# Kernel optimization log

Measured on AMD Instinct MI355X. Metric: run time of the kernel, lower is better.

## Reference

```python
import jax, jax.numpy as jnp
import numpy as np

NEG_INF = -1e9  # matches masked_fill value in torch code
LRELU_ALPHA = 0.2


def setup_inputs() -> dict:
    key = jax.random.key(0)
    k1, k2, k3, k4 = jax.random.split(key, 4)
    B, N, F_IN, H, DK = 4, 2048, 128, 4, 32
    x = jax.random.normal(k1, (B, N, F_IN), dtype=jnp.float32)
    adj = jax.random.randint(k2, (B, N, N), 0, 2, dtype=jnp.int32)
    # xavier-ish scaled params
    W = jax.random.normal(k3, (H, F_IN, DK), dtype=jnp.float32) * (1.0 / np.sqrt(F_IN))
    a = jax.random.normal(k4, (H, 2 * DK, 1), dtype=jnp.float32) * (1.0 / np.sqrt(2 * DK))
    return {"x": x, "adj": adj, "W": W, "a": a}


def reference(x, adj, W, a):
    B, N, _ = x.shape
    H, _, DK = W.shape
    # h: (B, H, N, DK)
    h = jnp.einsum('bni,hio->bhno', x, W)
    # Split attention vector: e[b,h,i,j] = h_i.a_l + h_j.a_r  (avoids O(N^2 * 2d) concat)
    a_l = a[:, :DK, 0]   # (H, DK)
    a_r = a[:, DK:, 0]   # (H, DK)
    el = jnp.einsum('bhnd,hd->bhn', h, a_l)  # (B, H, N)
    er = jnp.einsum('bhnd,hd->bhn', h, a_r)  # (B, H, N)
    e = el[:, :, :, None] + er[:, :, None, :]          # (B, H, N, N)
    e = jax.nn.leaky_relu(e, negative_slope=LRELU_ALPHA)
    e = jnp.where(adj[:, None, :, :] == 0, NEG_INF, e)
    alpha = jax.nn.softmax(e, axis=-1)                 # dropout is identity (eval)
    h_prime = jnp.einsum('bhij,bhjd->bhid', alpha, h)  # (B, H, N, DK)
    # torch code does h_prime.view(B, N, -1) on contiguous (B,H,N,DK): raw reshape
    out = h_prime.reshape(B, N, H * DK)
    return out
```

## Files before the change

### kernel.cpp

```cpp
#include <hip/hip_runtime.h>
#include <stdint.h>

#define LOG2E 1.4426950408889634f

typedef __bf16 v8bf __attribute__((ext_vector_type(8)));
typedef float v16f __attribute__((ext_vector_type(16)));

static constexpr int B = 4, N = 2048, FIN = 128, H = 4, DK = 32;
static constexpr int IT = N / 32;

__device__ __forceinline__ float exp2_fast(float x) {
#if __has_builtin(__builtin_amdgcn_exp2f)
  return __builtin_amdgcn_exp2f(x);
#else
  float r;
  asm("v_exp_f32 %0, %1" : "=v"(r) : "v"(x));
  return r;
#endif
}

__device__ __forceinline__ unsigned int bf16_rne(float f) {
  unsigned int u = __builtin_bit_cast(unsigned int, f);
  u += 0x7FFFu + ((u >> 16) & 1u);
  return u >> 16;
}

__global__ __launch_bounds__(256) void k_prep(const float* __restrict__ x,
                                              const float* __restrict__ W,
                                              unsigned short* __restrict__ xb,
                                              unsigned short* __restrict__ wtb) {
  int idx = blockIdx.x * 256 + threadIdx.x;
  constexpr int TX = B * N * FIN;
  if (idx < TX) {
    xb[idx] = (unsigned short)bf16_rne(x[idx]);
  } else {
    int j = idx - TX;
    int h = j >> 12, r = j & 4095, d = r >> 7, f = r & 127;
    wtb[j] = (unsigned short)bf16_rne(W[(h * FIN + f) * DK + d]);
  }
}

__global__ __launch_bounds__(256) void k_pack(const int* __restrict__ adj,
                                              unsigned int* __restrict__ adjb) {
  int wid = (blockIdx.x * 256 + threadIdx.x) >> 6;
  int lane = threadIdx.x & 63;
  const int* p = adj + (size_t)wid * 256 + lane;
  unsigned long long m0 = __ballot(p[0] != 0);
  unsigned long long m1 = __ballot(p[64] != 0);
  unsigned long long m2 = __ballot(p[128] != 0);
  unsigned long long m3 = __ballot(p[192] != 0);
  if (lane == 0) {
    uint4 v0 = {(unsigned)m0, (unsigned)(m0 >> 32), (unsigned)m1, (unsigned)(m1 >> 32)};
    uint4 v1 = {(unsigned)m2, (unsigned)(m2 >> 32), (unsigned)m3, (unsigned)(m3 >> 32)};
    uint4* dst = (uint4*)(adjb + (size_t)wid * 8);
    dst[0] = v0;
    dst[1] = v1;
  }
}

__global__ __launch_bounds__(256) void k_hproj(const unsigned short* __restrict__ xb,
                                               const unsigned short* __restrict__ wtb,
                                               const float* __restrict__ a,
                                               unsigned short* __restrict__ h_t,
                                               float* __restrict__ el,
                                               float* __restrict__ er) {
  int blk = blockIdx.x;
  int b = blk >> 6, it = blk & 63;
  int tid = threadIdx.x;
  int head = tid >> 6, lane = tid & 63;
  int lrow = lane & 31, kh = lane >> 5;
  int bh = b * H + head;
  int n = it * 32 + lrow;
  const unsigned short* xp = xb + (b * N + n) * FIN + kh * 8;
  const unsigned short* wp = wtb + (head * DK + lrow) * FIN + kh * 8;
  v16f acc = {};
#pragma unroll
  for (int s = 0; s < FIN / 16; ++s) {
    v8bf av = __builtin_bit_cast(v8bf, *(const int4*)(wp + s * 16));
    v8bf bv = __builtin_bit_cast(v8bf, *(const int4*)(xp + s * 16));
    acc = __builtin_amdgcn_mfma_f32_32x32x16_bf16(av, bv, acc, 0, 0, 0);
  }
  float pel = 0.f, per = 0.f;
#pragma unroll
  for (int r = 0; r < 16; ++r) {
    int d = (r & 3) + 8 * (r >> 2) + 4 * kh;
    float hv = acc[r];
    h_t[(bh * DK + d) * N + n] = (unsigned short)bf16_rne(hv);
    pel = fmaf(hv, a[head * 2 * DK + d], pel);
    per = fmaf(hv, a[head * 2 * DK + DK + d], per);
  }
  pel += __shfl_xor(pel, 32);
  per += __shfl_xor(per, 32);
  if (kh == 0) {
    el[bh * N + n] = pel * LOG2E;
    er[bh * N + n] = per * LOG2E;
  }
}

__global__ __launch_bounds__(1024, 4) void k_attn(const unsigned int* __restrict__ adjb,
                                                  const unsigned short* __restrict__ h_t,
                                                  const float* __restrict__ el,
                                                  const float* __restrict__ er,
                                                  float* __restrict__ out) {
  __shared__ float part[H][1024];
  __shared__ float lsh[H][32];
  int blk = blockIdx.x;
  int b = blk >> 6, it = blk & 63;
  int tid = threadIdx.x;
  int wave = tid >> 6;
  int head = wave & 3, jq = wave >> 2;
  int lane = tid & 63, lrow = lane & 31, kh = lane >> 5;
  int ig = it * 32 + lrow, bh = b * H + head;

  part[tid >> 8][tid & 255] = 0.f;
  part[tid >> 8][256 + (tid & 255)] = 0.f;
  part[tid >> 8][512 + (tid & 255)] = 0.f;
  part[tid >> 8][768 + (tid & 255)] = 0.f;
  if (tid < H * 32) lsh[tid >> 5][tid & 31] = 0.f;

  float eli = el[bh * N + ig];
  int j0 = jq * 512 + kh * 8;
  const float* erp = er + bh * N + j0;
  const unsigned short* hp = h_t + (size_t)(bh * DK + lrow) * N + j0;

  const uint4* abp = (const uint4*)(adjb + (size_t)(b * N + ig) * 64 + jq * 16);
  uint4 ab0 = abp[0], ab1 = abp[1], ab2 = abp[2], ab3 = abp[3];
  unsigned adw[16] = {ab0.x, ab0.y, ab0.z, ab0.w, ab1.x, ab1.y, ab1.z, ab1.w,
                      ab2.x, ab2.y, ab2.z, ab2.w, ab3.x, ab3.y, ab3.z, ab3.w};
  int shkh = kh * 8;

  __syncthreads();

  v16f acc = {};
  float lsum = 0.f;
  float4 Ea = *(const float4*)erp;
  float4 Eb = *(const float4*)(erp + 4);
  int4 Hb = *(const int4*)hp;
#pragma unroll
  for (int s = 0; s < 32; ++s) {
    float4 ea = Ea, eb = Eb;
    int4 hb = Hb;
    if (s + 1 < 32) {
      int o = (s + 1) * 16;
      Ea = *(const float4*)(erp + o);
      Eb = *(const float4*)(erp + o + 4);
      Hb = *(const int4*)(hp + o);
    }
    unsigned mb = (adw[s >> 1] >> (((s & 1) * 16) + shkh)) & 0xFFu;
    float ev[8] = {ea.x, ea.y, ea.z, ea.w, eb.x, eb.y, eb.z, eb.w};
    unsigned ub[8];
#pragma unroll
    for (int k = 0; k < 8; ++k) {
      float tt = eli + ev[k];
      tt = fmaxf(tt, 0.2f * tt);
      float pv = exp2_fast(tt);
      unsigned u = __builtin_bit_cast(unsigned, pv) & 0xFFFF0000u;
      u = (mb & (1u << k)) ? u : 0u;
      ub[k] = u;
      lsum += __builtin_bit_cast(float, u);
    }
    unsigned u0 = __builtin_amdgcn_perm(ub[1], ub[0], 0x07060302u);
    unsigned u1 = __builtin_amdgcn_perm(ub[3], ub[2], 0x07060302u);
    unsigned u2 = __builtin_amdgcn_perm(ub[5], ub[4], 0x07060302u);
    unsigned u3 = __builtin_amdgcn_perm(ub[7], ub[6], 0x07060302u);
    uint4 au = {u0, u1, u2, u3};
    v8bf av = __builtin_bit_cast(v8bf, au);
    v8bf hv = __builtin_bit_cast(v8bf, hb);
    acc = __builtin_amdgcn_mfma_f32_32x32x16_bf16(av, hv, acc, 0, 0, 0);
  }

  lsum += __shfl_xor(lsum, 32);
  if (lane < 32) atomicAdd(&lsh[head][lane], lsum);
#pragma unroll
  for (int r = 0; r < 16; ++r) {
    int rowl = (r & 3) + 8 * (r >> 2) + 4 * kh;
    atomicAdd(&part[head][rowl * 32 + lrow], acc[r]);
  }
  __syncthreads();

  int e = tid * 4;
  int rh = e >> 10;
  int ri = (e >> 5) & 31;
  int rd = e & 31;
  float4 s4 = *(const float4*)&part[rh][ri * 32 + rd];
  float inv = 1.0f / lsh[rh][ri];
  float4 o;
  o.x = s4.x * inv;
  o.y = s4.y * inv;
  o.z = s4.z * inv;
  o.w = s4.w * inv;
  *(float4*)&out[(size_t)((b * H + rh) * N + it * 32 + ri) * DK + rd] = o;
}

extern "C" void kernel_launch(void* const* d_in, const int* in_sizes, int n_in,
                              void* d_out, int out_size, void* d_ws, size_t ws_size,
                              hipStream_t stream) {
  const float* x = (const float*)d_in[0];
  const int* adj = (const int*)d_in[1];
  const float* W = (const float*)d_in[2];
  const float* a = (const float*)d_in[3];
  float* out = (float*)d_out;
  char* ws = (char*)d_ws;

  unsigned short* h_t = (unsigned short*)(ws);
  float* el = (float*)(ws + 0x200000);
  float* er = (float*)(ws + 0x220000);
  unsigned short* wtb = (unsigned short*)(ws + 0x240000);
  unsigned int* adjb = (unsigned int*)(ws + 0x250000);
  unsigned short* xb = (unsigned short*)(ws + 0x450000);

  hipLaunchKernelGGL(k_pack, dim3(B * N * N / 256 / 4), dim3(256), 0, stream, adj, adjb);
  hipLaunchKernelGGL(k_prep, dim3((B * N * FIN + H * DK * FIN) / 256), dim3(256), 0, stream,
                     x, W, xb, wtb);
  hipLaunchKernelGGL(k_hproj, dim3(B * IT), dim3(256), 0, stream, xb, wtb, a, h_t, el, er);
  hipLaunchKernelGGL(k_attn, dim3(B * IT), dim3(1024), 0, stream, adjb, h_t, el, er, out);
}
```

Baseline: 146.5 us.

## Fuse adjacency mask read into attention kernel and drop bit-packing pass

Removes the separate kernel that packed the int32 adjacency matrix into bitmasks. The attention kernel now reads raw adjacency rows itself, double-buffering them alongside the h tiles, and stages the per-head er vector in shared memory. Blocks shrink to 512 threads, so each wave covers 1024 columns. The two column-halves are combined with ordered shared-memory writes instead of LDS atomics. This saves one launch and the bitmask write/read round trip. In exchange, each block's four head waves load the same int32 adjacency rows separately, and more registers go to in-flight loads.

New measurement: 238.3 us. 62.7% more time.

```diff
diff --git a/kernel.cpp b/kernel.cpp
--- a/kernel.cpp
+++ b/kernel.cpp
@@ -37,24 +37,6 @@
     int j = idx - TX;
     int h = j >> 12, r = j & 4095, d = r >> 7, f = r & 127;
     wtb[j] = (unsigned short)bf16_rne(W[(h * FIN + f) * DK + d]);
-  }
-}
-
-__global__ __launch_bounds__(256) void k_pack(const int* __restrict__ adj,
-                                              unsigned int* __restrict__ adjb) {
-  int wid = (blockIdx.x * 256 + threadIdx.x) >> 6;
-  int lane = threadIdx.x & 63;
-  const int* p = adj + (size_t)wid * 256 + lane;
-  unsigned long long m0 = __ballot(p[0] != 0);
-  unsigned long long m1 = __ballot(p[64] != 0);
-  unsigned long long m2 = __ballot(p[128] != 0);
-  unsigned long long m3 = __ballot(p[192] != 0);
-  if (lane == 0) {
-    uint4 v0 = {(unsigned)m0, (unsigned)(m0 >> 32), (unsigned)m1, (unsigned)(m1 >> 32)};
-    uint4 v1 = {(unsigned)m2, (unsigned)(m2 >> 32), (unsigned)m3, (unsigned)(m3 >> 32)};
-    uint4* dst = (uint4*)(adjb + (size_t)wid * 8);
-    dst[0] = v0;
-    dst[1] = v1;
   }
 }
 
@@ -97,13 +79,14 @@
   }
 }
 
-__global__ __launch_bounds__(1024, 4) void k_attn(const unsigned int* __restrict__ adjb,
-                                                  const unsigned short* __restrict__ h_t,
-                                                  const float* __restrict__ el,
-                                                  const float* __restrict__ er,
-                                                  float* __restrict__ out) {
-  __shared__ float part[H][1024];
-  __shared__ float lsh[H][32];
+__global__ __launch_bounds__(512, 6) void k_attn(const int* __restrict__ adj,
+                                                 const unsigned short* __restrict__ h_t,
+                                                 const float* __restrict__ el,
+                                                 const float* __restrict__ er,
+                                                 float* __restrict__ out) {
+  __shared__ float ersh[H * N];
+  __shared__ float part[H * 1024];
+  __shared__ float lsh[H * 32];
   int blk = blockIdx.x;
   int b = blk >> 6, it = blk & 63;
   int tid = threadIdx.x;
@@ -112,41 +95,34 @@
   int lane = tid & 63, lrow = lane & 31, kh = lane >> 5;
   int ig = it * 32 + lrow, bh = b * H + head;
 
-  part[tid >> 8][tid & 255] = 0.f;
-  part[tid >> 8][256 + (tid & 255)] = 0.f;
-  part[tid >> 8][512 + (tid & 255)] = 0.f;
-  part[tid >> 8][768 + (tid & 255)] = 0.f;
-  if (tid < H * 32) lsh[tid >> 5][tid & 31] = 0.f;
+  {
+    const float4* esrc = (const float4*)(er + b * H * N);
+    float4* edst = (float4*)ersh;
+#pragma unroll
+    for (int r = 0; r < 4; ++r) edst[tid + r * 512] = esrc[tid + r * 512];
+  }
+  __syncthreads();
 
   float eli = el[bh * N + ig];
-  int j0 = jq * 512 + kh * 8;
-  const float* erp = er + bh * N + j0;
+  int j0 = jq * 1024 + kh * 8;
+  const int* arow = adj + (size_t)(b * N + ig) * N + j0;
   const unsigned short* hp = h_t + (size_t)(bh * DK + lrow) * N + j0;
-
-  const uint4* abp = (const uint4*)(adjb + (size_t)(b * N + ig) * 64 + jq * 16);
-  uint4 ab0 = abp[0], ab1 = abp[1], ab2 = abp[2], ab3 = abp[3];
-  unsigned adw[16] = {ab0.x, ab0.y, ab0.z, ab0.w, ab1.x, ab1.y, ab1.z, ab1.w,
-                      ab2.x, ab2.y, ab2.z, ab2.w, ab3.x, ab3.y, ab3.z, ab3.w};
-  int shkh = kh * 8;
-
-  __syncthreads();
+  const float* ep = ersh + head * N + j0;
 
   v16f acc = {};
   float lsum = 0.f;
-  float4 Ea = *(const float4*)erp;
-  float4 Eb = *(const float4*)(erp + 4);
-  int4 Hb = *(const int4*)hp;
-#pragma unroll
-  for (int s = 0; s < 32; ++s) {
-    float4 ea = Ea, eb = Eb;
-    int4 hb = Hb;
-    if (s + 1 < 32) {
-      int o = (s + 1) * 16;
-      Ea = *(const float4*)(erp + o);
-      Eb = *(const float4*)(erp + o + 4);
-      Hb = *(const int4*)(hp + o);
-    }
-    unsigned mb = (adw[s >> 1] >> (((s & 1) * 16) + shkh)) & 0xFFu;
+
+  int4 A0a = *(const int4*)(arow);
+  int4 A0b = *(const int4*)(arow + 4);
+  int4 H0 = *(const int4*)(hp);
+  int4 A1a = *(const int4*)(arow + 16);
+  int4 A1b = *(const int4*)(arow + 20);
+  int4 H1 = *(const int4*)(hp + 16);
+
+  auto step = [&](int4 aa, int4 ab, int4 hb, int s) {
+    float4 ea = *(const float4*)(ep + s * 16);
+    float4 eb = *(const float4*)(ep + s * 16 + 4);
+    int ad[8] = {aa.x, aa.y, aa.z, aa.w, ab.x, ab.y, ab.z, ab.w};
     float ev[8] = {ea.x, ea.y, ea.z, ea.w, eb.x, eb.y, eb.z, eb.w};
     unsigned ub[8];
 #pragma unroll
@@ -155,7 +131,7 @@
       tt = fmaxf(tt, 0.2f * tt);
       float pv = exp2_fast(tt);
       unsigned u = __builtin_bit_cast(unsigned, pv) & 0xFFFF0000u;
-      u = (mb & (1u << k)) ? u : 0u;
+      u = ad[k] ? u : 0u;
       ub[k] = u;
       lsum += __builtin_bit_cast(float, u);
     }
@@ -164,32 +140,63 @@
     unsigned u2 = __builtin_amdgcn_perm(ub[5], ub[4], 0x07060302u);
     unsigned u3 = __builtin_amdgcn_perm(ub[7], ub[6], 0x07060302u);
     uint4 au = {u0, u1, u2, u3};
-    v8bf av = __builtin_bit_cast(v8bf, au);
-    v8bf hv = __builtin_bit_cast(v8bf, hb);
-    acc = __builtin_amdgcn_mfma_f32_32x32x16_bf16(av, hv, acc, 0, 0, 0);
+    acc = __builtin_amdgcn_mfma_f32_32x32x16_bf16(
+        __builtin_bit_cast(v8bf, au), __builtin_bit_cast(v8bf, hb), acc, 0, 0, 0);
+  };
+
+#pragma unroll 4
+  for (int s = 0; s < 64; s += 2) {
+    int4 aa = A0a, ab = A0b, hb = H0;
+    if (s + 2 < 64) {
+      int o = (s + 2) * 16;
+      A0a = *(const int4*)(arow + o);
+      A0b = *(const int4*)(arow + o + 4);
+      H0 = *(const int4*)(hp + o);
+    }
+    step(aa, ab, hb, s);
+    aa = A1a; ab = A1b; hb = H1;
+    if (s + 3 < 64) {
+      int o = (s + 3) * 16;
+      A1a = *(const int4*)(arow + o);
+      A1b = *(const int4*)(arow + o + 4);
+      H1 = *(const int4*)(hp + o);
+    }
+    step(aa, ab, hb, s + 1);
   }
 
   lsum += __shfl_xor(lsum, 32);
-  if (lane < 32) atomicAdd(&lsh[head][lane], lsum);
-#pragma unroll
-  for (int r = 0; r < 16; ++r) {
-    int rowl = (r & 3) + 8 * (r >> 2) + 4 * kh;
-    atomicAdd(&part[head][rowl * 32 + lrow], acc[r]);
+
+  if (jq == 0) {
+    if (lane < 32) lsh[head * 32 + lane] = lsum;
+#pragma unroll
+    for (int r = 0; r < 16; ++r) {
+      int rowl = (r & 3) + 8 * (r >> 2) + 4 * kh;
+      part[head * 1024 + rowl * 32 + lrow] = acc[r];
+    }
   }
   __syncthreads();
-
-  int e = tid * 4;
+  if (jq == 1) {
+    if (lane < 32) lsh[head * 32 + lane] += lsum;
+#pragma unroll
+    for (int r = 0; r < 16; ++r) {
+      int rowl = (r & 3) + 8 * (r >> 2) + 4 * kh;
+      part[head * 1024 + rowl * 32 + lrow] += acc[r];
+    }
+  }
+  __syncthreads();
+
+  int e = tid * 8;
   int rh = e >> 10;
   int ri = (e >> 5) & 31;
   int rd = e & 31;
-  float4 s4 = *(const float4*)&part[rh][ri * 32 + rd];
-  float inv = 1.0f / lsh[rh][ri];
-  float4 o;
-  o.x = s4.x * inv;
-  o.y = s4.y * inv;
-  o.z = s4.z * inv;
-  o.w = s4.w * inv;
-  *(float4*)&out[(size_t)((b * H + rh) * N + it * 32 + ri) * DK + rd] = o;
+  float inv = 1.0f / lsh[rh * 32 + ri];
+  float4 s0 = *(const float4*)&part[rh * 1024 + ri * 32 + rd];
+  float4 s1 = *(const float4*)&part[rh * 1024 + ri * 32 + rd + 4];
+  float4 o0 = {s0.x * inv, s0.y * inv, s0.z * inv, s0.w * inv};
+  float4 o1 = {s1.x * inv, s1.y * inv, s1.z * inv, s1.w * inv};
+  float* op = out + (size_t)((b * H + rh) * N + it * 32 + ri) * DK + rd;
+  *(float4*)op = o0;
+  *(float4*)(op + 4) = o1;
 }
 
 extern "C" void kernel_launch(void* const* d_in, const int* in_sizes, int n_in,
@@ -206,12 +213,10 @@
   float* el = (float*)(ws + 0x200000);
   float* er = (float*)(ws + 0x220000);
   unsigned short* wtb = (unsigned short*)(ws + 0x240000);
-  unsigned int* adjb = (unsigned int*)(ws + 0x250000);
-  unsigned short* xb = (unsigned short*)(ws + 0x450000);
-
-  hipLaunchKernelGGL(k_pack, dim3(B * N * N / 256 / 4), dim3(256), 0, stream, adj, adjb);
+  unsigned short* xb = (unsigned short*)(ws + 0x250000);
+
   hipLaunchKernelGGL(k_prep, dim3((B * N * FIN + H * DK * FIN) / 256), dim3(256), 0, stream,
                      x, W, xb, wtb);
   hipLaunchKernelGGL(k_hproj, dim3(B * IT), dim3(256), 0, stream, xb, wtb, a, h_t, el, er);
-  hipLaunchKernelGGL(k_attn, dim3(B * IT), dim3(1024), 0, stream, adjb, h_t, el, er, out);
-}
+  hipLaunchKernelGGL(k_attn, dim3(B * IT), dim3(512), 0, stream, adj, h_t, el, er, out);
+}
```
